# Optimization experiments

Measured on AMD Instinct MI355X. Metric: run time of the kernel, lower is better.

## Reference

```python
import jax, jax.numpy as jnp
import numpy as np

MAX_RADIUS = 0.2
MIN_RADIUS = 0.0
SAMPLE_NUM = 32
CHANNEL = 64
EPS = 1e-5


def _ball_query(points, centers):
    """points (B,N,3), centers (B,M,3) -> idx (B,M,S) int32.
    Mimics pointnet2 ball_query: first SAMPLE_NUM point indices within
    [MIN_RADIUS, MAX_RADIUS); slots past the last found repeat the first
    found index (0 if the ball is empty)."""
    d2 = jnp.sum((centers[:, :, None, :] - points[:, None, :, :]) ** 2, axis=-1)  # (B,M,N)
    mask = (d2 < MAX_RADIUS ** 2) & (d2 >= MIN_RADIUS ** 2)
    N = points.shape[1]
    scores = jnp.where(mask, jnp.arange(N, dtype=jnp.int32), jnp.int32(N))
    neg_vals, _ = jax.lax.top_k(-scores, SAMPLE_NUM)  # k smallest indices
    idx = -neg_vals  # (B,M,S), invalid slots == N
    first = idx[..., :1]
    first = jnp.where(first == N, 0, first)
    idx = jnp.where(idx == N, first, idx)
    return idx


def setup_inputs() -> dict:
    key = jax.random.key(0)
    k1, k2, k3, k4 = jax.random.split(key, 4)
    B, N, M, C = 4, 16384, 2048, CHANNEL
    return {
        "points_xyz": jax.random.uniform(k1, (B, N, 3), dtype=jnp.float32),
        "center_xyz": jax.random.uniform(k2, (B, M, 3), dtype=jnp.float32),
        "center_feature": jax.random.normal(k3, (B, M, C), dtype=jnp.float32),
        "features": jax.random.normal(k4, (B, C, N), dtype=jnp.float32),
        "affine_alpha": jnp.ones((1, 1, 1, C + 3), dtype=jnp.float32),
        "affine_beta": jnp.zeros((1, 1, 1, C + 3), dtype=jnp.float32),
    }


def reference(points_xyz, center_xyz, center_feature, features, affine_alpha, affine_beta):
    idx = _ball_query(points_xyz, center_xyz)  # (B,M,S)
    gather = jax.vmap(lambda a, i: a[i])  # per-batch fancy gather
    grouped_xyz = gather(points_xyz, idx)                      # (B,M,S,3)
    grouped_feat = gather(jnp.swapaxes(features, 1, 2), idx)   # (B,M,S,C)
    nf = jnp.concatenate([grouped_xyz, grouped_feat], axis=-1)  # (B,M,S,3+C)
    mean = jnp.concatenate([center_xyz, center_feature], axis=-1)[:, :, None, :]
    centered = nf - mean
    B = nf.shape[0]
    # torch.std default: unbiased (ddof=1), one scalar per batch element
    std = jnp.std(centered.reshape(B, -1), axis=-1, ddof=1).reshape(B, 1, 1, 1)
    out = affine_alpha * (centered / (std + EPS)) + affine_beta  # (B,M,S,3+C)
    return jnp.transpose(out, (0, 3, 1, 2))  # (B,3+C,M,S)
```

## Files before the change

kernel.cpp:

```cpp
#include <hip/hip_runtime.h>
#include <cstdint>
#include <cstddef>

#define B_ 4
#define N_ 16384
#define M_ 2048
#define C_ 64
#define S_ 32
#define J_ 67
#define R2_ 0.04f
#define EPS_ 1e-5f

typedef float f32x4 __attribute__((ext_vector_type(4)));

__global__ __launch_bounds__(256) void k_phase1(
        const float* __restrict__ feat, float* __restrict__ featT,
        const float* __restrict__ pts, const float* __restrict__ ctr,
        int* __restrict__ idx_ws) {
    __shared__ float tile[64][65];
    int blk = blockIdx.x;
    int tid = threadIdx.x;

    if (blk >= 8192) {
        int ti = blk - 8192;
        int b  = ti >> 8;
        int n0 = (ti & 255) << 6;
        int r = tid >> 6, i = tid & 63;
        const float* fb = feat + (size_t)b * C_ * N_;
        #pragma unroll
        for (int cc = r; cc < 64; cc += 4)
            tile[cc][i] = __builtin_nontemporal_load(&fb[(size_t)cc * N_ + n0 + i]);
        __syncthreads();
        float* ftb = featT + (size_t)b * N_ * C_;
        #pragma unroll
        for (int nn = r; nn < 64; nn += 4)
            ftb[(size_t)(n0 + nn) * C_ + i] = tile[i][nn];
        return;
    }

    __shared__ int wcnt[4];
    __shared__ int widx[4][S_];
    __shared__ int result[S_];
    int w    = tid >> 6;
    int lane = tid & 63;
    int bm   = blk;
    int b    = bm >> 11;
    const float3* pb3 = (const float3*)(pts + (size_t)b * N_ * 3);
    float cx = ctr[(size_t)bm * 3 + 0];
    float cy = ctr[(size_t)bm * 3 + 1];
    float cz = ctr[(size_t)bm * 3 + 2];

    float3 cur[4], nxtv[4];
    #pragma unroll
    for (int r = 0; r < 4; r++)
        cur[r] = pb3[w * 256 + r * 64 + lane];
    int total = 0;
    for (int base = 0; base < N_; base += 1024) {
        int nb = base + 1024;
        if (nb < N_) {
            #pragma unroll
            for (int r = 0; r < 4; r++)
                nxtv[r] = pb3[nb + w * 256 + r * 64 + lane];
        }
        int cbase = base + w * 256;
        int cnt = 0;
        #pragma unroll
        for (int r = 0; r < 4; r++) {
            float dx = __fsub_rn(cx, cur[r].x);
            float dy = __fsub_rn(cy, cur[r].y);
            float dz = __fsub_rn(cz, cur[r].z);
            float d2 = __fadd_rn(__fadd_rn(__fmul_rn(dx, dx), __fmul_rn(dy, dy)),
                                 __fmul_rn(dz, dz));
            bool in = d2 < R2_;
            unsigned long long mk = __ballot(in);
            int rank = __popcll(mk & ((1ull << lane) - 1ull));
            int pos = cnt + rank;
            if (in && pos < S_) widx[w][pos] = cbase + r * 64 + lane;
            cnt += __popcll(mk);
        }
        if (lane == 0) wcnt[w] = cnt;
        __syncthreads();
        int c0 = wcnt[0], c1 = wcnt[1], c2 = wcnt[2], c3 = wcnt[3];
        int offw = total + ((w > 0) ? c0 : 0) + ((w > 1) ? c1 : 0) + ((w > 2) ? c2 : 0);
        int cw = wcnt[w] < S_ ? wcnt[w] : S_;
        if (lane < cw) {
            int dst = offw + lane;
            if (dst < S_) result[dst] = widx[w][lane];
        }
        __syncthreads();
        total += c0 + c1 + c2 + c3;
        if (total >= S_ || nb >= N_) break;
        #pragma unroll
        for (int r = 0; r < 4; r++) cur[r] = nxtv[r];
    }
    int cfound = total < S_ ? total : S_;
    if (tid < S_) {
        int first = (cfound > 0) ? result[0] : 0;
        int v = (tid < cfound) ? result[tid] : first;
        idx_ws[(size_t)bm * S_ + tid] = v;
    }
}

__global__ __launch_bounds__(256) void k_sums(
        const float* __restrict__ pts, const float* __restrict__ ctr,
        const float* __restrict__ featT, const float* __restrict__ cfeat,
        const int* __restrict__ idx_ws, float* __restrict__ bpart) {
    __shared__ float pp1[4], pp2[4];
    int w    = threadIdx.x >> 6;
    int lane = threadIdx.x & 63;
    int bm   = blockIdx.x * 4 + w;
    int b    = bm >> 11;
    const float3* pb3 = (const float3*)(pts + (size_t)b * N_ * 3);
    const float* ftb = featT + (size_t)b * N_ * C_;
    int id = idx_ws[(size_t)bm * S_ + (lane & 31)];
    float cf = cfeat[(size_t)bm * C_ + lane];
    float cx = ctr[(size_t)bm * 3 + 0];
    float cy = ctr[(size_t)bm * 3 + 1];
    float cz = ctr[(size_t)bm * 3 + 2];

    float s1 = 0.f, s2 = 0.f;
    float v[S_];
    #pragma unroll
    for (int s = 0; s < S_; s++) {
        int p = __shfl(id, s);
        v[s] = ftb[(size_t)p * C_ + lane];
    }
    #pragma unroll
    for (int s = 0; s < S_; s++) { float d = v[s] - cf; s1 += d; s2 += d * d; }
    float3 q = pb3[id];
    float cj = (lane < 32) ? cx : cy;
    float pv = (lane < 32) ? q.x : q.y;
    float d0 = pv - cj; s1 += d0; s2 += d0 * d0;
    if (lane < 32) { float dz = q.z - cz; s1 += dz; s2 += dz * dz; }
    #pragma unroll
    for (int off = 32; off > 0; off >>= 1) {
        s1 += __shfl_down(s1, off);
        s2 += __shfl_down(s2, off);
    }
    if (lane == 0) { pp1[w] = s1; pp2[w] = s2; }
    __syncthreads();
    if (threadIdx.x == 0) {
        bpart[blockIdx.x * 2 + 0] = ((pp1[0] + pp1[1]) + pp1[2]) + pp1[3];
        bpart[blockIdx.x * 2 + 1] = ((pp2[0] + pp2[1]) + pp2[2]) + pp2[3];
    }
}

__global__ __launch_bounds__(256) void k_output(
        const float* __restrict__ pts, const float* __restrict__ ctr,
        const float* __restrict__ featT, const float* __restrict__ cfeat,
        const float* __restrict__ alpha, const float* __restrict__ beta,
        const int* __restrict__ idx_ws, const float* __restrict__ bpart,
        float* __restrict__ out) {
    __shared__ float r1[256], r2[256];
    int blk = blockIdx.x, tid = threadIdx.x;
    int batch = blk >> 9;

    const float* bp = bpart + (size_t)batch * 512 * 2;
    r1[tid] = bp[tid * 2 + 0] + bp[(tid + 256) * 2 + 0];
    r2[tid] = bp[tid * 2 + 1] + bp[(tid + 256) * 2 + 1];
    __syncthreads();
    for (int off = 128; off > 0; off >>= 1) {
        if (tid < off) { r1[tid] += r1[tid + off]; r2[tid] += r2[tid + off]; }
        __syncthreads();
    }
    float sum = r1[0], sumsq = r2[0];
    const float n = (float)(M_ * S_ * J_);
    float mean = sum / n;
    float var  = (sumsq - sum * mean) / (n - 1.f);
    float inv  = 1.f / (sqrtf(var) + EPS_);

    int mi = tid >> 6;
    int cg = (tid >> 3) & 7;
    int sq = tid & 7;
    int m  = (blk & 511) * 4 + mi;
    int s0 = sq * 4;
    size_t bm = (size_t)batch * M_ + m;
    int4 pidx = *(const int4*)(idx_ws + bm * S_ + s0);
    size_t obase = ((size_t)batch * J_ * M_ + m) * (size_t)S_ + s0;

    if (cg == 0) {
        const float3* pb3 = (const float3*)(pts + (size_t)batch * N_ * 3);
        float3 q0 = pb3[pidx.x], q1 = pb3[pidx.y], q2 = pb3[pidx.z], q3 = pb3[pidx.w];
        float3 cj3;
        cj3.x = ctr[bm * 3 + 0]; cj3.y = ctr[bm * 3 + 1]; cj3.z = ctr[bm * 3 + 2];
        {
            float a = alpha[0] * inv, bt = beta[0];
            f32x4 o = { a * (q0.x - cj3.x) + bt, a * (q1.x - cj3.x) + bt,
                        a * (q2.x - cj3.x) + bt, a * (q3.x - cj3.x) + bt };
            __builtin_nontemporal_store(o, (f32x4*)(out + obase + (size_t)0 * (M_ * S_)));
        }
        {
            float a = alpha[1] * inv, bt = beta[1];
            f32x4 o = { a * (q0.y - cj3.y) + bt, a * (q1.y - cj3.y) + bt,
                        a * (q2.y - cj3.y) + bt, a * (q3.y - cj3.y) + bt };
            __builtin_nontemporal_store(o, (f32x4*)(out + obase + (size_t)1 * (M_ * S_)));
        }
        {
            float a = alpha[2] * inv, bt = beta[2];
            f32x4 o = { a * (q0.z - cj3.z) + bt, a * (q1.z - cj3.z) + bt,
                        a * (q2.z - cj3.z) + bt, a * (q3.z - cj3.z) + bt };
            __builtin_nontemporal_store(o, (f32x4*)(out + obase + (size_t)2 * (M_ * S_)));
        }
    }
    const float4* f0 = (const float4*)(featT + ((size_t)batch * N_ + pidx.x) * C_);
    const float4* f1 = (const float4*)(featT + ((size_t)batch * N_ + pidx.y) * C_);
    const float4* f2 = (const float4*)(featT + ((size_t)batch * N_ + pidx.z) * C_);
    const float4* f3 = (const float4*)(featT + ((size_t)batch * N_ + pidx.w) * C_);
    const float4* cf = (const float4*)(cfeat + bm * C_);
    #pragma unroll
    for (int cq = cg * 2; cq < cg * 2 + 2; cq++) {
        float4 v0 = f0[cq], v1 = f1[cq], v2 = f2[cq], v3 = f3[cq], c = cf[cq];
        int j = 3 + cq * 4;
        float a0 = alpha[j + 0] * inv, b0 = beta[j + 0];
        float a1 = alpha[j + 1] * inv, b1 = beta[j + 1];
        float a2 = alpha[j + 2] * inv, b2 = beta[j + 2];
        float a3 = alpha[j + 3] * inv, b3 = beta[j + 3];
        f32x4 o0, o1, o2, o3;
        o0.x = a0 * (v0.x - c.x) + b0; o0.y = a0 * (v1.x - c.x) + b0;
        o0.z = a0 * (v2.x - c.x) + b0; o0.w = a0 * (v3.x - c.x) + b0;
        o1.x = a1 * (v0.y - c.y) + b1; o1.y = a1 * (v1.y - c.y) + b1;
        o1.z = a1 * (v2.y - c.y) + b1; o1.w = a1 * (v3.y - c.y) + b1;
        o2.x = a2 * (v0.z - c.z) + b2; o2.y = a2 * (v1.z - c.z) + b2;
        o2.z = a2 * (v2.z - c.z) + b2; o2.w = a2 * (v3.z - c.z) + b2;
        o3.x = a3 * (v0.w - c.w) + b3; o3.y = a3 * (v1.w - c.w) + b3;
        o3.z = a3 * (v2.w - c.w) + b3; o3.w = a3 * (v3.w - c.w) + b3;
        __builtin_nontemporal_store(o0, (f32x4*)(out + obase + (size_t)(j + 0) * (M_ * S_)));
        __builtin_nontemporal_store(o1, (f32x4*)(out + obase + (size_t)(j + 1) * (M_ * S_)));
        __builtin_nontemporal_store(o2, (f32x4*)(out + obase + (size_t)(j + 2) * (M_ * S_)));
        __builtin_nontemporal_store(o3, (f32x4*)(out + obase + (size_t)(j + 3) * (M_ * S_)));
    }
}

extern "C" void kernel_launch(void* const* d_in, const int* in_sizes, int n_in,
                              void* d_out, int out_size, void* d_ws, size_t ws_size,
                              hipStream_t stream) {
    const float* pts   = (const float*)d_in[0];
    const float* ctr   = (const float*)d_in[1];
    const float* cfeat = (const float*)d_in[2];
    const float* feat  = (const float*)d_in[3];
    const float* alpha = (const float*)d_in[4];
    const float* beta  = (const float*)d_in[5];
    float* out = (float*)d_out;

    char* ws = (char*)d_ws;
    float* featT = (float*)ws;
    int*   idx_ws = (int*)(ws + (size_t)B_ * N_ * C_ * 4);
    float* bpart = (float*)(ws + (size_t)B_ * N_ * C_ * 4 + (size_t)B_ * M_ * S_ * 4);

    k_phase1<<<8192 + 1024, 256, 0, stream>>>(feat, featT, pts, ctr, idx_ws);
    k_sums<<<2048, 256, 0, stream>>>(pts, ctr, featT, cfeat, idx_ws, bpart);
    k_output<<<2048, 256, 0, stream>>>(pts, ctr, featT, cfeat, alpha, beta,
                                       idx_ws, bpart, out);
}
```

Before: 51.23 us.

## Reorder transpose blocks first, vectorize k_sums gathers, double per-block work in output

The feature-transpose blocks move to the front of the phase-1 grid and use normal cached loads instead of nontemporal ones, so featT is written early while the ball-query blocks run. k_sums now gathers float4 per lane (16 lanes per row, 4 samples per wavefront step), which cuts load instructions and register use. k_output processes 8 centers per block over half as many blocks, each thread handling 4 channel quads, so the per-block std reduction is amortized over more output. The trade-off is more work per thread and less parallelism in the output kernel.

After: 48.25 us. -5.8%, faster.

```diff
diff --git a/kernel.cpp b/kernel.cpp
--- a/kernel.cpp
+++ b/kernel.cpp
@@ -21,15 +21,14 @@
     int blk = blockIdx.x;
     int tid = threadIdx.x;
 
-    if (blk >= 8192) {
-        int ti = blk - 8192;
-        int b  = ti >> 8;
-        int n0 = (ti & 255) << 6;
+    if (blk < 1024) {
+        int b  = blk >> 8;
+        int n0 = (blk & 255) << 6;
         int r = tid >> 6, i = tid & 63;
         const float* fb = feat + (size_t)b * C_ * N_;
         #pragma unroll
         for (int cc = r; cc < 64; cc += 4)
-            tile[cc][i] = __builtin_nontemporal_load(&fb[(size_t)cc * N_ + n0 + i]);
+            tile[cc][i] = fb[(size_t)cc * N_ + n0 + i];
         __syncthreads();
         float* ftb = featT + (size_t)b * N_ * C_;
         #pragma unroll
@@ -43,7 +42,7 @@
     __shared__ int result[S_];
     int w    = tid >> 6;
     int lane = tid & 63;
-    int bm   = blk;
+    int bm   = blk - 1024;
     int b    = bm >> 11;
     const float3* pb3 = (const float3*)(pts + (size_t)b * N_ * 3);
     float cx = ctr[(size_t)bm * 3 + 0];
@@ -111,27 +110,36 @@
     int bm   = blockIdx.x * 4 + w;
     int b    = bm >> 11;
     const float3* pb3 = (const float3*)(pts + (size_t)b * N_ * 3);
-    const float* ftb = featT + (size_t)b * N_ * C_;
-    int id = idx_ws[(size_t)bm * S_ + (lane & 31)];
-    float cf = cfeat[(size_t)bm * C_ + lane];
+    const f32x4* ftb4 = (const f32x4*)(featT + (size_t)b * N_ * C_);
+    int sid = idx_ws[(size_t)bm * S_ + (lane & 31)];
+    int cq  = lane & 15;
+    f32x4 cf = ((const f32x4*)(cfeat + (size_t)bm * C_))[cq];
     float cx = ctr[(size_t)bm * 3 + 0];
     float cy = ctr[(size_t)bm * 3 + 1];
     float cz = ctr[(size_t)bm * 3 + 2];
 
+    f32x4 v[8];
+    #pragma unroll
+    for (int k = 0; k < 8; k++) {
+        int s = 4 * k + (lane >> 4);
+        int p = __shfl(sid, s);
+        v[k] = ftb4[(size_t)p * 16 + cq];
+    }
     float s1 = 0.f, s2 = 0.f;
-    float v[S_];
-    #pragma unroll
-    for (int s = 0; s < S_; s++) {
-        int p = __shfl(id, s);
-        v[s] = ftb[(size_t)p * C_ + lane];
-    }
-    #pragma unroll
-    for (int s = 0; s < S_; s++) { float d = v[s] - cf; s1 += d; s2 += d * d; }
-    float3 q = pb3[id];
-    float cj = (lane < 32) ? cx : cy;
-    float pv = (lane < 32) ? q.x : q.y;
-    float d0 = pv - cj; s1 += d0; s2 += d0 * d0;
-    if (lane < 32) { float dz = q.z - cz; s1 += dz; s2 += dz * dz; }
+    #pragma unroll
+    for (int k = 0; k < 8; k++) {
+        float d0 = v[k].x - cf.x, d1 = v[k].y - cf.y;
+        float d2 = v[k].z - cf.z, d3 = v[k].w - cf.w;
+        s1 += (d0 + d1) + (d2 + d3);
+        s2 += (d0 * d0 + d1 * d1) + (d2 * d2 + d3 * d3);
+    }
+    {
+        float3 q = pb3[sid];
+        float cj = (lane < 32) ? cx : cy;
+        float pv = (lane < 32) ? q.x : q.y;
+        float d0 = pv - cj; s1 += d0; s2 += d0 * d0;
+        if (lane < 32) { float dz = q.z - cz; s1 += dz; s2 += dz * dz; }
+    }
     #pragma unroll
     for (int off = 32; off > 0; off >>= 1) {
         s1 += __shfl_down(s1, off);
@@ -153,7 +161,7 @@
         float* __restrict__ out) {
     __shared__ float r1[256], r2[256];
     int blk = blockIdx.x, tid = threadIdx.x;
-    int batch = blk >> 9;
+    int batch = blk >> 8;
 
     const float* bp = bpart + (size_t)batch * 512 * 2;
     r1[tid] = bp[tid * 2 + 0] + bp[(tid + 256) * 2 + 0];
@@ -169,10 +177,10 @@
     float var  = (sumsq - sum * mean) / (n - 1.f);
     float inv  = 1.f / (sqrtf(var) + EPS_);
 
-    int mi = tid >> 6;
-    int cg = (tid >> 3) & 7;
+    int mi = tid >> 5;
+    int cg = (tid >> 3) & 3;
     int sq = tid & 7;
-    int m  = (blk & 511) * 4 + mi;
+    int m  = (blk & 255) * 8 + mi;
     int s0 = sq * 4;
     size_t bm = (size_t)batch * M_ + m;
     int4 pidx = *(const int4*)(idx_ws + bm * S_ + s0);
@@ -208,7 +216,7 @@
     const float4* f3 = (const float4*)(featT + ((size_t)batch * N_ + pidx.w) * C_);
     const float4* cf = (const float4*)(cfeat + bm * C_);
     #pragma unroll
-    for (int cq = cg * 2; cq < cg * 2 + 2; cq++) {
+    for (int cq = cg * 4; cq < cg * 4 + 4; cq++) {
         float4 v0 = f0[cq], v1 = f1[cq], v2 = f2[cq], v3 = f3[cq], c = cf[cq];
         int j = 3 + cq * 4;
         float a0 = alpha[j + 0] * inv, b0 = beta[j + 0];
@@ -247,8 +255,8 @@
     int*   idx_ws = (int*)(ws + (size_t)B_ * N_ * C_ * 4);
     float* bpart = (float*)(ws + (size_t)B_ * N_ * C_ * 4 + (size_t)B_ * M_ * S_ * 4);
 
-    k_phase1<<<8192 + 1024, 256, 0, stream>>>(feat, featT, pts, ctr, idx_ws);
+    k_phase1<<<1024 + B_ * M_, 256, 0, stream>>>(feat, featT, pts, ctr, idx_ws);
     k_sums<<<2048, 256, 0, stream>>>(pts, ctr, featT, cfeat, idx_ws, bpart);
-    k_output<<<2048, 256, 0, stream>>>(pts, ctr, featT, cfeat, alpha, beta,
+    k_output<<<1024, 256, 0, stream>>>(pts, ctr, featT, cfeat, alpha, beta,
                                        idx_ws, bpart, out);
 }
```
